# Kernel tuning notes

Measured on AMD Instinct MI355X. Metric: run time of the kernel, lower is better.

Reference implementation:

```python
import jax, jax.numpy as jnp
import numpy as np

NCOL = 22   # number of feature columns (hardcoded list in Virtue)
NEMB = 12   # embedding_num
D = 64      # embedding_dim
B = 2048    # batch size
REG = 1e-3  # reg coefficient from __init__


def setup_inputs() -> dict:
    key = jax.random.key(0)
    ks = jax.random.split(key, 8)
    features = jax.random.randint(ks[0], (NCOL, B), 0, NEMB, dtype=jnp.int32)
    tables = jax.random.normal(ks[1], (NCOL, NEMB, D), dtype=jnp.float32) * 0.1
    mlp_w1 = jax.random.normal(ks[2], (8,), dtype=jnp.float32) * 0.5   # Linear(1,8).weight
    mlp_b1 = jnp.zeros((8,), dtype=jnp.float32)
    mlp_w2 = jax.random.normal(ks[3], (8,), dtype=jnp.float32) * 0.5   # Linear(8,1).weight
    mlp_b2 = jnp.zeros((1,), dtype=jnp.float32)
    # FC weights: [plus, multiply, max, min] share input dim D; concat has 2D
    W_ops = jax.random.normal(ks[4], (4, NCOL, NCOL, 2, D), dtype=jnp.float32) / np.float32(np.sqrt(D))
    W_concat = jax.random.normal(ks[5], (NCOL, NCOL, 2, 2 * D), dtype=jnp.float32) / np.float32(np.sqrt(2 * D))
    # arch binary weights: ones/2 + 0.001*noise, as in _initialize_alphas
    arch_w = 0.5 + 0.001 * jax.random.normal(ks[6], (5,), dtype=jnp.float32)
    return dict(features=features, tables=tables, mlp_w1=mlp_w1, mlp_b1=mlp_b1,
                mlp_w2=mlp_w2, mlp_b2=mlp_b2, W_ops=W_ops, W_concat=W_concat,
                arch_w=arch_w)


def reference(features, tables, mlp_w1, mlp_b1, mlp_w2, mlp_b2, W_ops, W_concat, arch_w):
    # Embedding lookup for every column: E[i] = tables[i][features[i]] -> [22, B, D]
    E = tables[jnp.arange(NCOL)[:, None], features]
    col_norms = jnp.sqrt(jnp.sum(E * E, axis=(1, 2)))           # [22]
    regs = REG * (2.0 * NCOL) * jnp.sum(col_norms)
    # elementwise 1->8->1 MLP (mlp_p used for BOTH sides, as in original code)
    h = jnp.tanh(E[..., None] * mlp_w1 + mlp_b1)                # [22, B, D, 8]
    trans = jnp.einsum('ibdh,h->ibd', h, mlp_w2) + mlp_b2[0]    # [22, B, D]
    Wp, Wm, Wmax, Wmin = W_ops[0], W_ops[1], W_ops[2], W_ops[3]
    # plus: sum_ij (p_i+q_j) W_ij^T decomposes into two small contractions
    out_plus = (jnp.einsum('ibd,iod->bo', trans, Wp.sum(1))
                + jnp.einsum('jbd,jod->bo', trans, Wp.sum(0)))
    # multiply: sum_ij sum_d p_id q_jd W_ijod, two-step to avoid [22,22,B,D]
    tmp = jnp.einsum('ibd,ijod->bjod', trans, Wm)               # [B, 22, 2, D]
    out_mul = jnp.einsum('bjod,jbd->bo', tmp, trans)
    # max/min: genuinely pairwise elementwise nonlinearity
    pq_max = jnp.maximum(trans[:, None], trans[None, :])        # [22, 22, B, D]
    out_max = jnp.einsum('ijbd,ijod->bo', pq_max, Wmax)
    pq_min = jnp.minimum(trans[:, None], trans[None, :])
    out_min = jnp.einsum('ijbd,ijod->bo', pq_min, Wmin)
    # concat: fc([p;q]) = p Wc1^T + q Wc2^T, decomposes like plus
    Wc1, Wc2 = W_concat[..., :D], W_concat[..., D:]
    out_cat = (jnp.einsum('ibd,iod->bo', trans, Wc1.sum(1))
               + jnp.einsum('jbd,jod->bo', trans, Wc2.sum(0)))
    inferences = (arch_w[0] * out_plus + arch_w[1] * out_mul + arch_w[2] * out_max
                  + arch_w[3] * out_min + arch_w[4] * out_cat)   # [B, 2]
    return inferences, regs
```

## Files before the change

### kernel.cpp

```cpp
#include <hip/hip_runtime.h>
#include <math.h>

#define NCOL 22
#define NEMB 12
#define D 64
#define BB 2048
#define NUP 253
#define REGC 0.001f

__device__ __forceinline__ float ftanh(float x) {
    float cx = fminf(fmaxf(x, -10.f), 10.f);
    float e = __expf(2.f * cx);
    return (e - 1.f) / (e + 1.f);
}

__device__ __forceinline__ void up_ij(int p, int& io, int& jo) {
    int s = 0, i = 0, j = 0;
    #pragma unroll
    for (int k = 0; k < NCOL; ++k) {
        int rl = NCOL - k;
        if (p >= s && p < s + rl) { i = k; j = k + (p - s); }
        s += rl;
    }
    io = i; jo = j;
}

__global__ __launch_bounds__(768) void k_build(
    const int* __restrict__ features, const float* __restrict__ tables,
    const float* __restrict__ w1, const float* __restrict__ b1,
    const float* __restrict__ w2, const float* __restrict__ b2,
    const float* __restrict__ W_ops, const float* __restrict__ W_concat,
    const float* __restrict__ aw,
    float2* __restrict__ ptab2, float* __restrict__ cn)
{
    int bid = blockIdx.x, tid = threadIdx.x;

    if (bid >= 2 * NUP) {
        int i = bid - 2 * NUP;
        __shared__ float ssq[NEMB];
        __shared__ float parts[12];
        if (tid < NEMB) {
            const float* tp = tables + (i * NEMB + tid) * D;
            float s = 0.f;
            #pragma unroll
            for (int d = 0; d < D; ++d) s = fmaf(tp[d], tp[d], s);
            ssq[tid] = s;
        }
        __syncthreads();
        float s = 0.f;
        for (int k = tid; k < BB; k += 768) s += ssq[features[i * BB + k]];
        #pragma unroll
        for (int m = 32; m; m >>= 1) s += __shfl_xor(s, m);
        if ((tid & 63) == 0) parts[tid >> 6] = s;
        __syncthreads();
        if (tid == 0) {
            float t = 0.f;
            #pragma unroll
            for (int q = 0; q < 12; ++q) t += parts[q];
            cn[i] = sqrtf(t);
        }
        return;
    }

    int pair = bid >> 1, h = bid & 1;
    int i, j;
    up_ij(pair, i, j);
    bool diag = (i == j);
    int dbase = h * 32;

    __shared__ float ti[NEMB][33];
    __shared__ float tj[NEMB][33];
    __shared__ float4 w4s[32];
    __shared__ float wls[2][32];
    __shared__ float2 comb[144][4];

    float b2v = b2[0];
    float a0 = aw[0], a1 = aw[1], a2 = aw[2], a3 = aw[3], a4 = aw[4];
    const float* Wm   = W_ops + 1 * NCOL * NCOL * 2 * D;
    const float* Wmax = W_ops + 2 * NCOL * NCOL * 2 * D;
    const float* Wmin = W_ops + 3 * NCOL * NCOL * 2 * D;

    {
        int k = tid;
        int half = (k >= NEMB * 32);
        int kk = k - half * NEMB * 32;
        int e = kk >> 5, dd = kk & 31;
        float x = tables[(half ? j : i) * NEMB * D + e * D + dbase + dd];
        float acc = b2v;
        #pragma unroll
        for (int hh = 0; hh < 8; ++hh)
            acc = fmaf(ftanh(fmaf(x, w1[hh], b1[hh])), w2[hh], acc);
        (half ? tj : ti)[e][dd] = acc;
    }

    if (tid < 32) {
        int d = dbase + tid;
        int pij = i * NCOL + j, pji = j * NCOL + i;
        int a_ij = (pij * 2 + 0) * D + d, b_ij = (pij * 2 + 1) * D + d;
        float4 v;
        if (diag) {
            v.x = a1 * Wm[a_ij];
            v.y = a1 * Wm[b_ij];
            v.z = 0.5f * (a2 * Wmax[a_ij] - a3 * Wmin[a_ij]);
            v.w = 0.5f * (a2 * Wmax[b_ij] - a3 * Wmin[b_ij]);
        } else {
            int a_ji = (pji * 2 + 0) * D + d, b_ji = (pji * 2 + 1) * D + d;
            v.x = a1 * (Wm[a_ij] + Wm[a_ji]);
            v.y = a1 * (Wm[b_ij] + Wm[b_ji]);
            v.z = 0.5f * (a2 * (Wmax[a_ij] + Wmax[a_ji])
                        - a3 * (Wmin[a_ij] + Wmin[a_ji]));
            v.w = 0.5f * (a2 * (Wmax[b_ij] + Wmax[b_ji])
                        - a3 * (Wmin[b_ij] + Wmin[b_ji]));
        }
        w4s[tid] = v;
    }

    if (diag && tid >= 64 && tid < 128) {
        int t = tid - 64;
        int o = t >> 5, dd = t & 31;
        int d = dbase + dd;
        float lp = 0.f, lc = 0.f, lmm = 0.f;
        #pragma unroll
        for (int jj = 0; jj < NCOL; ++jj) {
            int ij = ((i * NCOL + jj) * 2 + o) * D + d;
            int ji = ((jj * NCOL + i) * 2 + o) * D + d;
            lp += W_ops[ij] + W_ops[ji];
            lc += W_concat[((i * NCOL + jj) * 2 + o) * 2 * D + d]
                + W_concat[((jj * NCOL + i) * 2 + o) * 2 * D + D + d];
            lmm += a2 * (Wmax[ij] + Wmax[ji]) + a3 * (Wmin[ij] + Wmin[ji]);
        }
        wls[o][dd] = a0 * lp + a4 * lc + 0.5f * lmm;
    }
    __syncthreads();

    if (tid < 576) {
        int c = tid >> 2, sub = tid & 3;
        int ei = c / NEMB, ej = c - (c / NEMB) * NEMB;
        int d0 = sub * 8;
        bool dl = diag & (ei == ej);
        float r0 = 0.f, r1 = 0.f, l0 = 0.f, l1 = 0.f;
        #pragma unroll
        for (int dd = d0; dd < d0 + 8; ++dd) {
            float a = ti[ei][dd], b = tj[ej][dd];
            float4 w4 = w4s[dd];
            float pp = a * b, dfa = fabsf(a - b);
            r0 = fmaf(pp, w4.x, fmaf(dfa, w4.z, r0));
            r1 = fmaf(pp, w4.y, fmaf(dfa, w4.w, r1));
            if (dl) {
                l0 = fmaf(a, wls[0][dd], l0);
                l1 = fmaf(a, wls[1][dd], l1);
            }
        }
        comb[c][sub] = make_float2(r0 + l0, r1 + l1);
    }
    __syncthreads();
    if (tid < 144) {
        float2 u0 = comb[tid][0], u1 = comb[tid][1];
        float2 u2 = comb[tid][2], u3 = comb[tid][3];
        ptab2[(pair * 144 + tid) * 2 + h] =
            make_float2(u0.x + u1.x + u2.x + u3.x,
                        u0.y + u1.y + u2.y + u3.y);
    }
}

__global__ __launch_bounds__(256) void k_gather(const int* __restrict__ features,
        const float4* __restrict__ ptab4, const float* __restrict__ cn,
        float* __restrict__ out)
{
    __shared__ int fs[NCOL][4];
    __shared__ float red[4][4][2];
    __shared__ int lip[NUP], ljp[NUP];
    int tid = threadIdx.x;
    int b0 = blockIdx.x * 4;

    for (int p = tid; p < NUP; p += 256) {
        int ii, jj;
        up_ij(p, ii, jj);
        lip[p] = ii; ljp[p] = jj;
    }
    if (tid >= 256 - NCOL * 4) {
        int k = tid - (256 - NCOL * 4);
        int i = k >> 2, q = k & 3;
        fs[i][q] = features[i * BB + b0 + q];
    }
    __syncthreads();

    int b = tid & 3, g = tid >> 2;
    int p0 = (g * NUP) >> 6, p1 = ((g + 1) * NUP) >> 6;
    float a0 = 0.f, a1 = 0.f;
    #pragma unroll 2
    for (int p = p0; p < p1; ++p) {
        float4 v = ptab4[p * 144 + fs[lip[p]][b] * NEMB + fs[ljp[p]][b]];
        a0 += v.x + v.z;
        a1 += v.y + v.w;
    }
    #pragma unroll
    for (int m = 4; m <= 32; m <<= 1) {
        a0 += __shfl_xor(a0, m);
        a1 += __shfl_xor(a1, m);
    }
    int w = tid >> 6, lane = tid & 63;
    if (lane < 4) {
        red[w][lane][0] = a0;
        red[w][lane][1] = a1;
    }
    __syncthreads();
    if (tid < 8) {
        int bb = tid >> 1, o = tid & 1;
        out[(b0 + bb) * 2 + o] = red[0][bb][o] + red[1][bb][o]
                               + red[2][bb][o] + red[3][bb][o];
    }
    if (blockIdx.x == 0 && tid == 64) {
        float s = 0.f;
        for (int c = 0; c < NCOL; ++c) s += cn[c];
        out[BB * 2] = REGC * (2.0f * NCOL) * s;
    }
}

extern "C" void kernel_launch(void* const* d_in, const int* in_sizes, int n_in,
                              void* d_out, int out_size, void* d_ws, size_t ws_size,
                              hipStream_t stream) {
    const int*   features = (const int*)d_in[0];
    const float* tables   = (const float*)d_in[1];
    const float* w1       = (const float*)d_in[2];
    const float* b1       = (const float*)d_in[3];
    const float* w2       = (const float*)d_in[4];
    const float* b2       = (const float*)d_in[5];
    const float* W_ops    = (const float*)d_in[6];
    const float* W_concat = (const float*)d_in[7];
    const float* aw       = (const float*)d_in[8];
    float* out = (float*)d_out;
    char*  ws  = (char*)d_ws;

    float2* ptab2 = (float2*)ws;
    float*  cn    = (float*)(ws + 582912);

    k_build <<<dim3(2 * NUP + NCOL), dim3(768), 0, stream>>>(
        features, tables, w1, b1, w2, b2, W_ops, W_concat, aw, ptab2, cn);
    k_gather<<<dim3(512), dim3(256), 0, stream>>>(
        features, (const float4*)ws, cn, out);
}
```

Before: 18.14 us.

## Parallelize diagonal weight fold, closed-form pair index, pack column norms

Several changes at once. The diagonal-block weight fold over 22 columns is spread across 704 threads and reduced through shared memory, replacing a 64-thread serial loop. The pair-index decode now uses a closed-form sqrt instead of a 22-step loop, so the gather kernel computes it inline and drops its shared lookup tables. Column-norm blocks now handle 4 columns each, cutting the build grid to 512 blocks. The tanh divide becomes a hardware reciprocal. The float sqrt decode has off-by-one correction steps that must hold at boundaries, and the new fold array adds shared memory per block.

```diff
diff --git a/kernel.cpp b/kernel.cpp
--- a/kernel.cpp
+++ b/kernel.cpp
@@ -11,18 +11,15 @@
 __device__ __forceinline__ float ftanh(float x) {
     float cx = fminf(fmaxf(x, -10.f), 10.f);
     float e = __expf(2.f * cx);
-    return (e - 1.f) / (e + 1.f);
+    return (e - 1.f) * __builtin_amdgcn_rcpf(e + 1.f);
 }
 
 __device__ __forceinline__ void up_ij(int p, int& io, int& jo) {
-    int s = 0, i = 0, j = 0;
-    #pragma unroll
-    for (int k = 0; k < NCOL; ++k) {
-        int rl = NCOL - k;
-        if (p >= s && p < s + rl) { i = k; j = k + (p - s); }
-        s += rl;
-    }
-    io = i; jo = j;
+    int i = (int)((45.0f - sqrtf(2025.0f - 8.0f * (float)p)) * 0.5f);
+    int s = (i * (45 - i)) >> 1;
+    if (p < s)                 { --i; s = (i * (45 - i)) >> 1; }
+    else if (p - s >= NCOL - i){ ++i; s = (i * (45 - i)) >> 1; }
+    io = i; jo = i + (p - s);
 }
 
 __global__ __launch_bounds__(768) void k_build(
@@ -36,29 +33,29 @@
     int bid = blockIdx.x, tid = threadIdx.x;
 
     if (bid >= 2 * NUP) {
-        int i = bid - 2 * NUP;
-        __shared__ float ssq[NEMB];
-        __shared__ float parts[12];
-        if (tid < NEMB) {
-            const float* tp = tables + (i * NEMB + tid) * D;
+        int cb = bid - 2 * NUP;
+        int grp = tid / 192, lt = tid - grp * 192;
+        int col = cb * 4 + grp;
+        __shared__ float ssq4[4][NEMB];
+        __shared__ float parts[4][3];
+        if (col < NCOL && lt < NEMB) {
+            const float* tp = tables + (col * NEMB + lt) * D;
             float s = 0.f;
             #pragma unroll
             for (int d = 0; d < D; ++d) s = fmaf(tp[d], tp[d], s);
-            ssq[tid] = s;
+            ssq4[grp][lt] = s;
         }
         __syncthreads();
-        float s = 0.f;
-        for (int k = tid; k < BB; k += 768) s += ssq[features[i * BB + k]];
-        #pragma unroll
-        for (int m = 32; m; m >>= 1) s += __shfl_xor(s, m);
-        if ((tid & 63) == 0) parts[tid >> 6] = s;
+        if (col < NCOL) {
+            float s = 0.f;
+            for (int k = lt; k < BB; k += 192) s += ssq4[grp][features[col * BB + k]];
+            #pragma unroll
+            for (int m = 32; m; m >>= 1) s += __shfl_xor(s, m);
+            if ((lt & 63) == 0) parts[grp][lt >> 6] = s;
+        }
         __syncthreads();
-        if (tid == 0) {
-            float t = 0.f;
-            #pragma unroll
-            for (int q = 0; q < 12; ++q) t += parts[q];
-            cn[i] = sqrtf(t);
-        }
+        if (col < NCOL && lt == 0)
+            cn[col] = sqrtf(parts[grp][0] + parts[grp][1] + parts[grp][2]);
         return;
     }
 
@@ -73,6 +70,7 @@
     __shared__ float4 w4s[32];
     __shared__ float wls[2][32];
     __shared__ float2 comb[144][4];
+    __shared__ float fold[NCOL][2][32];
 
     float b2v = b2[0];
     float a0 = aw[0], a1 = aw[1], a2 = aw[2], a3 = aw[3], a4 = aw[4];
@@ -115,23 +113,32 @@
         w4s[tid] = v;
     }
 
-    if (diag && tid >= 64 && tid < 128) {
-        int t = tid - 64;
-        int o = t >> 5, dd = t & 31;
+    if (diag && tid < NCOL * 32) {
+        int jj = tid >> 5, dd = tid & 31;
         int d = dbase + dd;
-        float lp = 0.f, lc = 0.f, lmm = 0.f;
         #pragma unroll
-        for (int jj = 0; jj < NCOL; ++jj) {
+        for (int o = 0; o < 2; ++o) {
             int ij = ((i * NCOL + jj) * 2 + o) * D + d;
             int ji = ((jj * NCOL + i) * 2 + o) * D + d;
-            lp += W_ops[ij] + W_ops[ji];
-            lc += W_concat[((i * NCOL + jj) * 2 + o) * 2 * D + d]
-                + W_concat[((jj * NCOL + i) * 2 + o) * 2 * D + D + d];
-            lmm += a2 * (Wmax[ij] + Wmax[ji]) + a3 * (Wmin[ij] + Wmin[ji]);
-        }
-        wls[o][dd] = a0 * lp + a4 * lc + 0.5f * lmm;
-    }
-    __syncthreads();
+            float lp = W_ops[ij] + W_ops[ji];
+            float lc = W_concat[((i * NCOL + jj) * 2 + o) * 2 * D + d]
+                     + W_concat[((jj * NCOL + i) * 2 + o) * 2 * D + D + d];
+            float lmm = a2 * (Wmax[ij] + Wmax[ji]) + a3 * (Wmin[ij] + Wmin[ji]);
+            fold[jj][o][dd] = a0 * lp + a4 * lc + 0.5f * lmm;
+        }
+    }
+    __syncthreads();
+
+    if (diag) {
+        if (tid < 64) {
+            int o = tid >> 5, dd = tid & 31;
+            float s = 0.f;
+            #pragma unroll
+            for (int jj = 0; jj < NCOL; ++jj) s += fold[jj][o][dd];
+            wls[o][dd] = s;
+        }
+        __syncthreads();
+    }
 
     if (tid < 576) {
         int c = tid >> 2, sub = tid & 3;
@@ -169,18 +176,11 @@
 {
     __shared__ int fs[NCOL][4];
     __shared__ float red[4][4][2];
-    __shared__ int lip[NUP], ljp[NUP];
     int tid = threadIdx.x;
     int b0 = blockIdx.x * 4;
 
-    for (int p = tid; p < NUP; p += 256) {
-        int ii, jj;
-        up_ij(p, ii, jj);
-        lip[p] = ii; ljp[p] = jj;
-    }
-    if (tid >= 256 - NCOL * 4) {
-        int k = tid - (256 - NCOL * 4);
-        int i = k >> 2, q = k & 3;
+    if (tid < NCOL * 4) {
+        int i = tid >> 2, q = tid & 3;
         fs[i][q] = features[i * BB + b0 + q];
     }
     __syncthreads();
@@ -190,7 +190,9 @@
     float a0 = 0.f, a1 = 0.f;
     #pragma unroll 2
     for (int p = p0; p < p1; ++p) {
-        float4 v = ptab4[p * 144 + fs[lip[p]][b] * NEMB + fs[ljp[p]][b]];
+        int ii, jj;
+        up_ij(p, ii, jj);
+        float4 v = ptab4[p * 144 + fs[ii][b] * NEMB + fs[jj][b]];
         a0 += v.x + v.z;
         a1 += v.y + v.w;
     }
@@ -235,7 +237,7 @@
     float2* ptab2 = (float2*)ws;
     float*  cn    = (float*)(ws + 582912);
 
-    k_build <<<dim3(2 * NUP + NCOL), dim3(768), 0, stream>>>(
+    k_build <<<dim3(512), dim3(768), 0, stream>>>(
         features, tables, w1, b1, w2, b2, W_ops, W_concat, aw, ptab2, cn);
     k_gather<<<dim3(512), dim3(256), 0, stream>>>(
         features, (const float4*)ws, cn, out);
```

Measured after the change: 14.85 us. 18.1% less time.
